# Performance work log

Hardware: AMD Instinct MI355X
Metric: run time of the kernel (lower is better)

Reference implementation:

```python
import jax, jax.numpy as jnp
import numpy as np

BN_EPS = 1e-5

def _conv1x1(w, b, x):
    # w: (O, C), b: (O,), x: (B, C, T) -> (B, O, T)
    return jnp.einsum('oc,bct->bot', w, x) + b[None, :, None]

def _maxpool2(x):
    # MaxPool1d(kernel_size=2, stride=2): (B, C, T) -> (B, C, T//2)
    B, C, T = x.shape
    return x.reshape(B, C, T // 2, 2).max(axis=-1)

def setup_inputs() -> dict:
    key = jax.random.key(0)
    ks = jax.random.split(key, 11)
    B, C, Ci, T = 4, 256, 128, 8192
    s_in = 1.0 / np.sqrt(C)
    s_ic = 1.0 / np.sqrt(Ci)
    return {
        'x':       jax.random.normal(ks[0], (B, C, T), dtype=jnp.float32),
        'theta_w': jax.random.uniform(ks[1], (Ci, C), jnp.float32, -s_in, s_in),
        'theta_b': jax.random.uniform(ks[2], (Ci,),   jnp.float32, -s_in, s_in),
        'phi_w':   jax.random.uniform(ks[3], (Ci, C), jnp.float32, -s_in, s_in),
        'phi_b':   jax.random.uniform(ks[4], (Ci,),   jnp.float32, -s_in, s_in),
        'g_w':     jax.random.uniform(ks[5], (Ci, C), jnp.float32, -s_in, s_in),
        'g_b':     jax.random.uniform(ks[6], (Ci,),   jnp.float32, -s_in, s_in),
        'w_w':     jax.random.uniform(ks[7], (C, Ci), jnp.float32, -s_ic, s_ic),
        'w_b':     jax.random.uniform(ks[8], (C,),    jnp.float32, -s_ic, s_ic),
        'gamma':   jax.random.normal(ks[9], (C,), dtype=jnp.float32),
        'beta':    jax.random.normal(ks[10], (C,), dtype=jnp.float32),
    }

def reference(x, theta_w, theta_b, phi_w, phi_b, g_w, g_b, w_w, w_b, gamma, beta):
    # x: (B, C, T)
    theta = _conv1x1(theta_w, theta_b, x)            # (B, Ci, T)
    phi   = _maxpool2(_conv1x1(phi_w, phi_b, x))     # (B, Ci, N), N = T//2
    g     = _maxpool2(_conv1x1(g_w, g_b, x))         # (B, Ci, N)
    N = phi.shape[-1]
    # f = theta^T phi / N  (dot-product similarity, divide-by-N normalization)
    f = jnp.einsum('bct,bcn->btn', theta, phi) / N   # (B, T, N)
    y = jnp.einsum('btn,bcn->bct', f, g)             # (B, Ci, T)
    wy = _conv1x1(w_w, w_b, y)                       # (B, C, T)
    # BatchNorm1d (training mode: batch statistics over (B, T), biased var)
    mean = wy.mean(axis=(0, 2), keepdims=True)
    var = ((wy - mean) ** 2).mean(axis=(0, 2), keepdims=True)
    bn = gamma[None, :, None] * (wy - mean) * jax.lax.rsqrt(var + BN_EPS) + beta[None, :, None]
    return bn + x
```

## Files before the change

### kernel.cpp

```cpp
#include <hip/hip_runtime.h>
#include <hip/hip_bf16.h>


constexpr int B = 4, C = 256, CI = 128, T = 8192, N = 4096;
constexpr int TT = 128;
constexpr int OT = 64;
constexpr int KC = 32;

constexpr size_t OFF_PHI = 0;
constexpr size_t OFF_G   = OFF_PHI + (size_t)B*CI*N;
constexpr size_t OFF_S   = OFF_G   + (size_t)B*CI*N;
constexpr size_t OFF_M   = OFF_S   + (size_t)B*CI*CI;
constexpr size_t OFF_W2  = OFF_M   + (size_t)B*C*CI;
constexpr size_t OFF_B2  = OFF_W2  + (size_t)B*C*C;
constexpr size_t OFF_WY  = OFF_B2  + (size_t)B*C;
constexpr size_t OFF_SUM = OFF_WY  + (size_t)B*C*T;
constexpr size_t OFF_A   = OFF_SUM + 2*(size_t)C;
constexpr size_t OFF_SH  = OFF_A   + (size_t)C;

__global__ __launch_bounds__(256) void k1_convpool(
    const float* __restrict__ x, const float* __restrict__ phi_w,
    const float* __restrict__ phi_b, const float* __restrict__ g_w,
    const float* __restrict__ g_b, float* __restrict__ phi_pool,
    float* __restrict__ g_pool)
{
    int t0 = blockIdx.x * TT;
    int ro = blockIdx.y * OT;
    int b  = blockIdx.z;

    __shared__ float ws_w[OT][KC];
    __shared__ float xs[KC][TT];

    int tid = threadIdx.x;
    int tx = tid & 31, ty = tid >> 5;
    float acc[8][4];
    #pragma unroll
    for (int j = 0; j < 8; ++j)
        #pragma unroll
        for (int i = 0; i < 4; ++i) acc[j][i] = 0.f;

    const float* xb = x + (size_t)b * C * T;

    for (int c0 = 0; c0 < C; c0 += KC) {
        #pragma unroll
        for (int l = 0; l < 8; ++l) {
            int li = tid + l * 256;
            int r = li >> 5, k = li & 31;
            int row = ro + r;
            ws_w[r][k] = (row < CI) ? phi_w[(size_t)row * C + c0 + k]
                                    : g_w[(size_t)(row - CI) * C + c0 + k];
        }
        #pragma unroll
        for (int l = 0; l < 16; ++l) {
            int li = tid + l * 256;
            int k = li >> 7, t = li & 127;
            xs[k][t] = xb[(size_t)(c0 + k) * T + t0 + t];
        }
        __syncthreads();
        for (int k = 0; k < KC; k += 4) {
            float4 xv0 = *reinterpret_cast<const float4*>(&xs[k + 0][tx * 4]);
            float4 xv1 = *reinterpret_cast<const float4*>(&xs[k + 1][tx * 4]);
            float4 xv2 = *reinterpret_cast<const float4*>(&xs[k + 2][tx * 4]);
            float4 xv3 = *reinterpret_cast<const float4*>(&xs[k + 3][tx * 4]);
            #pragma unroll
            for (int j = 0; j < 8; ++j) {
                float4 wv = *reinterpret_cast<const float4*>(&ws_w[ty * 8 + j][k]);
                acc[j][0] += wv.x * xv0.x; acc[j][0] += wv.y * xv1.x;
                acc[j][0] += wv.z * xv2.x; acc[j][0] += wv.w * xv3.x;
                acc[j][1] += wv.x * xv0.y; acc[j][1] += wv.y * xv1.y;
                acc[j][1] += wv.z * xv2.y; acc[j][1] += wv.w * xv3.y;
                acc[j][2] += wv.x * xv0.z; acc[j][2] += wv.y * xv1.z;
                acc[j][2] += wv.z * xv2.z; acc[j][2] += wv.w * xv3.z;
                acc[j][3] += wv.x * xv0.w; acc[j][3] += wv.y * xv1.w;
                acc[j][3] += wv.z * xv2.w; acc[j][3] += wv.w * xv3.w;
            }
        }
        __syncthreads();
    }
    int n0 = (t0 >> 1) + tx * 2;
    #pragma unroll
    for (int j = 0; j < 8; ++j) {
        int row = ro + ty * 8 + j;
        float m0 = fmaxf(acc[j][0], acc[j][1]);
        float m1 = fmaxf(acc[j][2], acc[j][3]);
        if (row < CI) {
            float bias = phi_b[row];
            float2 v = {m0 + bias, m1 + bias};
            *reinterpret_cast<float2*>(&phi_pool[((size_t)b * CI + row) * N + n0]) = v;
        } else {
            float bias = g_b[row - CI];
            float2 v = {m0 + bias, m1 + bias};
            *reinterpret_cast<float2*>(&g_pool[((size_t)b * CI + (row - CI)) * N + n0]) = v;
        }
    }
}

__global__ __launch_bounds__(256) void k2_S(
    const float* __restrict__ phi_pool, const float* __restrict__ g_pool,
    float* __restrict__ S)
{
    int n0 = blockIdx.x * 128;
    int b  = blockIdx.y;
    __shared__ float gs[CI][33];
    __shared__ float ps[CI][33];
    int tid = threadIdx.x;
    int jg = tid & 15, ig = tid >> 4;
    float acc[8][8] = {};
    const float* gp = g_pool + (size_t)b * CI * N;
    const float* pp = phi_pool + (size_t)b * CI * N;
    for (int ks = 0; ks < 128; ks += 32) {
        #pragma unroll
        for (int l = 0; l < 16; ++l) {
            int li = tid + l * 256;
            int r = li >> 5, k = li & 31;
            gs[r][k] = gp[(size_t)r * N + n0 + ks + k];
            ps[r][k] = pp[(size_t)r * N + n0 + ks + k];
        }
        __syncthreads();
        for (int k = 0; k < 32; ++k) {
            float gv[8], pv[8];
            #pragma unroll
            for (int u = 0; u < 8; ++u) gv[u] = gs[ig + 16 * u][k];
            #pragma unroll
            for (int v = 0; v < 8; ++v) pv[v] = ps[jg + 16 * v][k];
            #pragma unroll
            for (int u = 0; u < 8; ++u)
                #pragma unroll
                for (int v = 0; v < 8; ++v) acc[u][v] += gv[u] * pv[v];
        }
        __syncthreads();
    }
    #pragma unroll
    for (int u = 0; u < 8; ++u) {
        int i = ig + 16 * u;
        #pragma unroll
        for (int v = 0; v < 8; ++v) {
            int j = jg + 16 * v;
            atomicAdd(&S[((size_t)b * CI + i) * CI + j], acc[u][v]);
        }
    }
}

__global__ __launch_bounds__(256) void k3a_M(
    const float* __restrict__ w_w, const float* __restrict__ S,
    float* __restrict__ M)
{
    int idx = blockIdx.x * 256 + threadIdx.x;
    int j = idx & (CI - 1);
    int r = (idx >> 7) & (C - 1);
    int b = idx >> 15;
    const float* Sb = S + (size_t)b * CI * CI;
    float a = 0.f;
    for (int k = 0; k < CI; ++k) a += w_w[(size_t)r * CI + k] * Sb[(size_t)k * CI + j];
    M[idx] = a * (1.f / N);
}

__global__ __launch_bounds__(256) void k3b_W2(
    const float* __restrict__ M, const float* __restrict__ theta_w,
    const float* __restrict__ theta_b, const float* __restrict__ w_b,
    float* __restrict__ W2, float* __restrict__ b2)
{
    int idx = blockIdx.x * 256 + threadIdx.x;
    int c = idx & (C - 1);
    int r = (idx >> 8) & (C - 1);
    int b = idx >> 16;
    const float* Mb = M + ((size_t)b * C + r) * CI;
    float a = 0.f;
    for (int k = 0; k < CI; ++k) a += Mb[k] * theta_w[(size_t)k * C + c];
    W2[idx] = a;
    if (c == 0) {
        float bv = 0.f;
        for (int k = 0; k < CI; ++k) bv += Mb[k] * theta_b[k];
        b2[(size_t)b * C + r] = bv + w_b[r];
    }
}

__global__ __launch_bounds__(256) void k4_conv2(
    const float* __restrict__ x, const float* __restrict__ W2,
    const float* __restrict__ b2, float* __restrict__ wy,
    float* __restrict__ gsum, float* __restrict__ gsq)
{
    int t0 = blockIdx.x * TT;
    int ro = blockIdx.y * OT;
    int b  = blockIdx.z;

    __shared__ float ws_w[OT][KC];
    __shared__ float xs[KC][TT];

    int tid = threadIdx.x;
    int tx = tid & 31, ty = tid >> 5;
    float acc[8][4];
    #pragma unroll
    for (int j = 0; j < 8; ++j)
        #pragma unroll
        for (int i = 0; i < 4; ++i) acc[j][i] = 0.f;

    const float* xb  = x + (size_t)b * C * T;
    const float* W2b = W2 + (size_t)b * C * C;

    for (int c0 = 0; c0 < C; c0 += KC) {
        #pragma unroll
        for (int l = 0; l < 8; ++l) {
            int li = tid + l * 256;
            int r = li >> 5, k = li & 31;
            ws_w[r][k] = W2b[(size_t)(ro + r) * C + c0 + k];
        }
        #pragma unroll
        for (int l = 0; l < 16; ++l) {
            int li = tid + l * 256;
            int k = li >> 7, t = li & 127;
            xs[k][t] = xb[(size_t)(c0 + k) * T + t0 + t];
        }
        __syncthreads();
        for (int k = 0; k < KC; k += 4) {
            float4 xv0 = *reinterpret_cast<const float4*>(&xs[k + 0][tx * 4]);
            float4 xv1 = *reinterpret_cast<const float4*>(&xs[k + 1][tx * 4]);
            float4 xv2 = *reinterpret_cast<const float4*>(&xs[k + 2][tx * 4]);
            float4 xv3 = *reinterpret_cast<const float4*>(&xs[k + 3][tx * 4]);
            #pragma unroll
            for (int j = 0; j < 8; ++j) {
                float4 wv = *reinterpret_cast<const float4*>(&ws_w[ty * 8 + j][k]);
                acc[j][0] += wv.x * xv0.x; acc[j][0] += wv.y * xv1.x;
                acc[j][0] += wv.z * xv2.x; acc[j][0] += wv.w * xv3.x;
                acc[j][1] += wv.x * xv0.y; acc[j][1] += wv.y * xv1.y;
                acc[j][1] += wv.z * xv2.y; acc[j][1] += wv.w * xv3.y;
                acc[j][2] += wv.x * xv0.z; acc[j][2] += wv.y * xv1.z;
                acc[j][2] += wv.z * xv2.z; acc[j][2] += wv.w * xv3.z;
                acc[j][3] += wv.x * xv0.w; acc[j][3] += wv.y * xv1.w;
                acc[j][3] += wv.z * xv2.w; acc[j][3] += wv.w * xv3.w;
            }
        }
        __syncthreads();
    }
    #pragma unroll
    for (int j = 0; j < 8; ++j) {
        int row = ro + ty * 8 + j;
        float bias = b2[(size_t)b * C + row];
        float4 v;
        v.x = acc[j][0] + bias; v.y = acc[j][1] + bias;
        v.z = acc[j][2] + bias; v.w = acc[j][3] + bias;
        *reinterpret_cast<float4*>(&wy[((size_t)b * C + row) * T + t0 + tx * 4]) = v;
        float ls = v.x + v.y + v.z + v.w;
        float lq = v.x * v.x + v.y * v.y + v.z * v.z + v.w * v.w;
        #pragma unroll
        for (int m = 16; m >= 1; m >>= 1) {
            ls += __shfl_xor(ls, m, 32);
            lq += __shfl_xor(lq, m, 32);
        }
        if (tx == 0) {
            atomicAdd(&gsum[row], ls);
            atomicAdd(&gsq[row], lq);
        }
    }
}

__global__ void k4b_stats(const float* __restrict__ gsum, const float* __restrict__ gsq,
                          const float* __restrict__ gamma, const float* __restrict__ beta,
                          float* __restrict__ a, float* __restrict__ sh)
{
    int c = threadIdx.x;
    const float invBT = 1.f / (float)(B * T);
    float mean = gsum[c] * invBT;
    float var  = gsq[c] * invBT - mean * mean;
    float av = gamma[c] * rsqrtf(var + 1e-5f);
    a[c]  = av;
    sh[c] = beta[c] - av * mean;
}

__global__ __launch_bounds__(256) void k5_bn(
    const float* __restrict__ x, const float* __restrict__ wy,
    const float* __restrict__ a, const float* __restrict__ sh,
    float* __restrict__ out)
{
    size_t total4 = (size_t)B * C * T / 4;
    for (size_t i = (size_t)blockIdx.x * blockDim.x + threadIdx.x; i < total4;
         i += (size_t)gridDim.x * blockDim.x) {
        size_t e = i * 4;
        int c = (int)((e / T) % C);
        float4 w4 = reinterpret_cast<const float4*>(wy)[i];
        float4 x4 = reinterpret_cast<const float4*>(x)[i];
        float av = a[c], sv = sh[c];
        float4 o;
        o.x = av * w4.x + sv + x4.x;
        o.y = av * w4.y + sv + x4.y;
        o.z = av * w4.z + sv + x4.z;
        o.w = av * w4.w + sv + x4.w;
        reinterpret_cast<float4*>(out)[i] = o;
    }
}

extern "C" void kernel_launch(void* const* d_in, const int* in_sizes, int n_in,
                              void* d_out, int out_size, void* d_ws, size_t ws_size,
                              hipStream_t stream)
{
    const float* x       = (const float*)d_in[0];
    const float* theta_w = (const float*)d_in[1];
    const float* theta_b = (const float*)d_in[2];
    const float* phi_w   = (const float*)d_in[3];
    const float* phi_b   = (const float*)d_in[4];
    const float* g_w     = (const float*)d_in[5];
    const float* g_b     = (const float*)d_in[6];
    const float* w_w     = (const float*)d_in[7];
    const float* w_b     = (const float*)d_in[8];
    const float* gamma   = (const float*)d_in[9];
    const float* beta    = (const float*)d_in[10];
    float* out = (float*)d_out;
    float* ws  = (float*)d_ws;

    float* phi_pool = ws + OFF_PHI;
    float* g_pool   = ws + OFF_G;
    float* Sbuf     = ws + OFF_S;
    float* Mbuf     = ws + OFF_M;
    float* W2buf    = ws + OFF_W2;
    float* b2buf    = ws + OFF_B2;
    float* wybuf    = ws + OFF_WY;
    float* gsum     = ws + OFF_SUM;
    float* gsq      = gsum + C;
    float* abuf     = ws + OFF_A;
    float* shbuf    = ws + OFF_SH;

    hipMemsetAsync(Sbuf, 0, (size_t)B * CI * CI * sizeof(float), stream);
    hipMemsetAsync(gsum, 0, 2 * (size_t)C * sizeof(float), stream);

    k1_convpool<<<dim3(T / TT, C / OT, B), 256, 0, stream>>>(
        x, phi_w, phi_b, g_w, g_b, phi_pool, g_pool);
    k2_S<<<dim3(N / 128, B), 256, 0, stream>>>(phi_pool, g_pool, Sbuf);
    k3a_M<<<(B * C * CI) / 256, 256, 0, stream>>>(w_w, Sbuf, Mbuf);
    k3b_W2<<<(B * C * C) / 256, 256, 0, stream>>>(Mbuf, theta_w, theta_b, w_b, W2buf, b2buf);
    k4_conv2<<<dim3(T / TT, C / OT, B), 256, 0, stream>>>(
        x, W2buf, b2buf, wybuf, gsum, gsq);
    k4b_stats<<<1, C, 0, stream>>>(gsum, gsq, gamma, beta, abuf, shbuf);
    k5_bn<<<2048, 256, 0, stream>>>(x, wybuf, abuf, shbuf, out);
}
```

Before: 299.9 us.

## Move 1x1 convs and Gram matrix to bf16x3 split MFMA with recomputed output

Replaces the FP32 FMA GEMMs (conv+pool, phi·g Gram reduction, final conv) with MFMA bf16 instructions, using a hi/lo bf16 split and three MFMAs per product to keep near-FP32 accuracy. x is transposed and split once into bf16 hi/lo in a pre-pass, and the pooled phi/g outputs are stored the same way. The wy intermediate is removed: the final conv runs twice, first to gather BN statistics and then again to apply BN and the residual directly to the output. This trades redundant MFMA work and an extra split pass for fewer FP32 ALU cycles and less wy global traffic.

```diff
diff --git a/kernel.cpp b/kernel.cpp
--- a/kernel.cpp
+++ b/kernel.cpp
@@ -2,148 +2,230 @@
 #include <hip/hip_bf16.h>
 
 
-constexpr int B = 4, C = 256, CI = 128, T = 8192, N = 4096;
-constexpr int TT = 128;
-constexpr int OT = 64;
-constexpr int KC = 32;
-
-constexpr size_t OFF_PHI = 0;
-constexpr size_t OFF_G   = OFF_PHI + (size_t)B*CI*N;
-constexpr size_t OFF_S   = OFF_G   + (size_t)B*CI*N;
-constexpr size_t OFF_M   = OFF_S   + (size_t)B*CI*CI;
-constexpr size_t OFF_W2  = OFF_M   + (size_t)B*C*CI;
-constexpr size_t OFF_B2  = OFF_W2  + (size_t)B*C*C;
-constexpr size_t OFF_WY  = OFF_B2  + (size_t)B*C;
-constexpr size_t OFF_SUM = OFF_WY  + (size_t)B*C*T;
-constexpr size_t OFF_A   = OFF_SUM + 2*(size_t)C;
-constexpr size_t OFF_SH  = OFF_A   + (size_t)C;
-
-__global__ __launch_bounds__(256) void k1_convpool(
-    const float* __restrict__ x, const float* __restrict__ phi_w,
-    const float* __restrict__ phi_b, const float* __restrict__ g_w,
-    const float* __restrict__ g_b, float* __restrict__ phi_pool,
-    float* __restrict__ g_pool)
-{
-    int t0 = blockIdx.x * TT;
-    int ro = blockIdx.y * OT;
-    int b  = blockIdx.z;
-
-    __shared__ float ws_w[OT][KC];
-    __shared__ float xs[KC][TT];
-
+constexpr int B = 4, C = 256, CI = 128, T = 8192, NN = 4096;
+
+using s16x8 = __attribute__((ext_vector_type(8))) short;
+using f32x4 = __attribute__((ext_vector_type(4))) float;
+
+__device__ __forceinline__ unsigned short f2bf(float f) {
+    unsigned int x = __float_as_uint(f);
+    unsigned int r = (x + 0x7fffu + ((x >> 16) & 1u)) >> 16;
+    return (unsigned short)r;
+}
+__device__ __forceinline__ float bf2f(unsigned short u) {
+    return __uint_as_float((unsigned int)u << 16);
+}
+
+#define MFMA(a, b, c) __builtin_amdgcn_mfma_f32_16x16x32_bf16((a), (b), (c), 0, 0, 0)
+
+constexpr size_t SZ_XT = (size_t)B * T * C * 2;
+constexpr size_t O_XTH = 0;
+constexpr size_t O_XTL = O_XTH + SZ_XT;
+constexpr size_t O_WSH = O_XTL + SZ_XT;
+constexpr size_t O_WSL = O_WSH + (size_t)C * C * 2;
+constexpr size_t SZ_P  = (size_t)B * CI * NN * 2;
+constexpr size_t O_PH  = O_WSL + (size_t)C * C * 2;
+constexpr size_t O_PL  = O_PH + SZ_P;
+constexpr size_t O_GH  = O_PL + SZ_P;
+constexpr size_t O_GL  = O_GH + SZ_P;
+constexpr size_t O_S   = O_GL + SZ_P;
+constexpr size_t O_M   = O_S  + (size_t)B * CI * CI * 4;
+constexpr size_t O_W2H = O_M  + (size_t)B * C * CI * 4;
+constexpr size_t O_W2L = O_W2H + (size_t)B * C * C * 2;
+constexpr size_t O_B2  = O_W2L + (size_t)B * C * C * 2;
+constexpr size_t O_GS  = O_B2 + (size_t)B * C * 4;
+constexpr size_t O_GQ  = O_GS + (size_t)C * 4;
+constexpr size_t O_A   = O_GQ + (size_t)C * 4;
+constexpr size_t O_SH  = O_A  + (size_t)C * 4;
+
+__global__ __launch_bounds__(256) void k0_split(
+    const float* __restrict__ x, unsigned short* __restrict__ xth,
+    unsigned short* __restrict__ xtl)
+{
+    __shared__ float xs[64][65];
+    int t0 = blockIdx.x * 64, c0 = blockIdx.y * 64, b = blockIdx.z;
     int tid = threadIdx.x;
-    int tx = tid & 31, ty = tid >> 5;
-    float acc[8][4];
-    #pragma unroll
-    for (int j = 0; j < 8; ++j)
-        #pragma unroll
-        for (int i = 0; i < 4; ++i) acc[j][i] = 0.f;
-
     const float* xb = x + (size_t)b * C * T;
-
-    for (int c0 = 0; c0 < C; c0 += KC) {
-        #pragma unroll
-        for (int l = 0; l < 8; ++l) {
-            int li = tid + l * 256;
-            int r = li >> 5, k = li & 31;
-            int row = ro + r;
-            ws_w[r][k] = (row < CI) ? phi_w[(size_t)row * C + c0 + k]
-                                    : g_w[(size_t)(row - CI) * C + c0 + k];
-        }
-        #pragma unroll
-        for (int l = 0; l < 16; ++l) {
-            int li = tid + l * 256;
-            int k = li >> 7, t = li & 127;
-            xs[k][t] = xb[(size_t)(c0 + k) * T + t0 + t];
-        }
-        __syncthreads();
-        for (int k = 0; k < KC; k += 4) {
-            float4 xv0 = *reinterpret_cast<const float4*>(&xs[k + 0][tx * 4]);
-            float4 xv1 = *reinterpret_cast<const float4*>(&xs[k + 1][tx * 4]);
-            float4 xv2 = *reinterpret_cast<const float4*>(&xs[k + 2][tx * 4]);
-            float4 xv3 = *reinterpret_cast<const float4*>(&xs[k + 3][tx * 4]);
-            #pragma unroll
-            for (int j = 0; j < 8; ++j) {
-                float4 wv = *reinterpret_cast<const float4*>(&ws_w[ty * 8 + j][k]);
-                acc[j][0] += wv.x * xv0.x; acc[j][0] += wv.y * xv1.x;
-                acc[j][0] += wv.z * xv2.x; acc[j][0] += wv.w * xv3.x;
-                acc[j][1] += wv.x * xv0.y; acc[j][1] += wv.y * xv1.y;
-                acc[j][1] += wv.z * xv2.y; acc[j][1] += wv.w * xv3.y;
-                acc[j][2] += wv.x * xv0.z; acc[j][2] += wv.y * xv1.z;
-                acc[j][2] += wv.z * xv2.z; acc[j][2] += wv.w * xv3.z;
-                acc[j][3] += wv.x * xv0.w; acc[j][3] += wv.y * xv1.w;
-                acc[j][3] += wv.z * xv2.w; acc[j][3] += wv.w * xv3.w;
+    #pragma unroll
+    for (int p = 0; p < 4; ++p) {
+        int idx = tid + p * 256;
+        int cr = idx >> 4;
+        int tg = (idx & 15) * 4;
+        float4 v = *reinterpret_cast<const float4*>(xb + (size_t)(c0 + cr) * T + t0 + tg);
+        xs[tg + 0][cr] = v.x; xs[tg + 1][cr] = v.y;
+        xs[tg + 2][cr] = v.z; xs[tg + 3][cr] = v.w;
+    }
+    __syncthreads();
+    #pragma unroll
+    for (int p = 0; p < 2; ++p) {
+        int idx = tid + p * 256;
+        int cg = idx & 7, tl = idx >> 3;
+        s16x8 hs, ls;
+        #pragma unroll
+        for (int j = 0; j < 8; ++j) {
+            float v = xs[tl][cg * 8 + j];
+            unsigned short h = f2bf(v);
+            unsigned short l = f2bf(v - bf2f(h));
+            hs[j] = (short)h; ls[j] = (short)l;
+        }
+        size_t dst = ((size_t)b * T + t0 + tl) * C + c0 + cg * 8;
+        *reinterpret_cast<s16x8*>(xth + dst) = hs;
+        *reinterpret_cast<s16x8*>(xtl + dst) = ls;
+    }
+}
+
+__global__ __launch_bounds__(256) void k0w(
+    const float* __restrict__ phi_w, const float* __restrict__ g_w,
+    unsigned short* __restrict__ wsh, unsigned short* __restrict__ wsl)
+{
+    int idx = blockIdx.x * 256 + threadIdx.x;
+    int row = idx >> 8, c = idx & 255;
+    float v = (row < CI) ? phi_w[(size_t)row * C + c] : g_w[(size_t)(row - CI) * C + c];
+    unsigned short h = f2bf(v);
+    wsh[idx] = h;
+    wsl[idx] = f2bf(v - bf2f(h));
+}
+
+__global__ __launch_bounds__(512) void k1_mfma(
+    const unsigned short* __restrict__ xth, const unsigned short* __restrict__ xtl,
+    const unsigned short* __restrict__ wsh, const unsigned short* __restrict__ wsl,
+    const float* __restrict__ phi_b, const float* __restrict__ g_b,
+    unsigned short* __restrict__ ph, unsigned short* __restrict__ pl,
+    unsigned short* __restrict__ gh, unsigned short* __restrict__ gl)
+{
+    int b = blockIdx.y, t0 = blockIdx.x * 128;
+    int tid = threadIdx.x, lane = tid & 63, w = tid >> 6;
+    int wo = w & 3, th = w >> 2;
+    int lr = lane & 15, lk = lane >> 4;
+
+    f32x4 acc[4][4];
+    #pragma unroll
+    for (int i = 0; i < 4; ++i)
+        #pragma unroll
+        for (int j = 0; j < 4; ++j) acc[i][j] = (f32x4){0.f, 0.f, 0.f, 0.f};
+
+    const unsigned short* ah_b = xth + ((size_t)b * T + t0 + th * 64 + lr) * C + lk * 8;
+    const unsigned short* al_b = xtl + ((size_t)b * T + t0 + th * 64 + lr) * C + lk * 8;
+    const unsigned short* bh_b = wsh + (size_t)(wo * 64 + lr) * C + lk * 8;
+    const unsigned short* bl_b = wsl + (size_t)(wo * 64 + lr) * C + lk * 8;
+
+    for (int c0 = 0; c0 < C; c0 += 32) {
+        s16x8 Ah[4], Al[4], Bh[4], Bl[4];
+        #pragma unroll
+        for (int ts = 0; ts < 4; ++ts) {
+            Ah[ts] = *reinterpret_cast<const s16x8*>(ah_b + (size_t)ts * 16 * C + c0);
+            Al[ts] = *reinterpret_cast<const s16x8*>(al_b + (size_t)ts * 16 * C + c0);
+        }
+        #pragma unroll
+        for (int os = 0; os < 4; ++os) {
+            Bh[os] = *reinterpret_cast<const s16x8*>(bh_b + (size_t)os * 16 * C + c0);
+            Bl[os] = *reinterpret_cast<const s16x8*>(bl_b + (size_t)os * 16 * C + c0);
+        }
+        #pragma unroll
+        for (int os = 0; os < 4; ++os)
+            #pragma unroll
+            for (int ts = 0; ts < 4; ++ts) {
+                acc[os][ts] = MFMA(Ah[ts], Bh[os], acc[os][ts]);
+                acc[os][ts] = MFMA(Al[ts], Bh[os], acc[os][ts]);
+                acc[os][ts] = MFMA(Ah[ts], Bl[os], acc[os][ts]);
             }
-        }
-        __syncthreads();
-    }
-    int n0 = (t0 >> 1) + tx * 2;
-    #pragma unroll
-    for (int j = 0; j < 8; ++j) {
-        int row = ro + ty * 8 + j;
-        float m0 = fmaxf(acc[j][0], acc[j][1]);
-        float m1 = fmaxf(acc[j][2], acc[j][3]);
-        if (row < CI) {
-            float bias = phi_b[row];
-            float2 v = {m0 + bias, m1 + bias};
-            *reinterpret_cast<float2*>(&phi_pool[((size_t)b * CI + row) * N + n0]) = v;
-        } else {
-            float bias = g_b[row - CI];
-            float2 v = {m0 + bias, m1 + bias};
-            *reinterpret_cast<float2*>(&g_pool[((size_t)b * CI + (row - CI)) * N + n0]) = v;
-        }
-    }
-}
-
-__global__ __launch_bounds__(256) void k2_S(
-    const float* __restrict__ phi_pool, const float* __restrict__ g_pool,
+    }
+
+    __shared__ unsigned int pool_s[256][65];
+    #pragma unroll
+    for (int os = 0; os < 4; ++os) {
+        int o = wo * 64 + os * 16 + lr;
+        float bias = (o < CI) ? phi_b[o] : g_b[o - CI];
+        #pragma unroll
+        for (int ts = 0; ts < 4; ++ts) {
+            f32x4 v = acc[os][ts];
+            float m0 = fmaxf(v[0], v[1]) + bias;
+            float m1 = fmaxf(v[2], v[3]) + bias;
+            int nl = th * 32 + ts * 8 + lk * 2;
+            unsigned short h0 = f2bf(m0), h1 = f2bf(m1);
+            unsigned int u0 = (unsigned int)h0 | ((unsigned int)f2bf(m0 - bf2f(h0)) << 16);
+            unsigned int u1 = (unsigned int)h1 | ((unsigned int)f2bf(m1 - bf2f(h1)) << 16);
+            pool_s[o][nl] = u0;
+            pool_s[o][nl + 1] = u1;
+        }
+    }
+    __syncthreads();
+    int o = tid >> 1, hf = tid & 1;
+    size_t n0 = (size_t)(t0 >> 1) + hf * 32;
+    unsigned short* dh = (o < CI ? ph + ((size_t)b * CI + o) * NN
+                                 : gh + ((size_t)b * CI + o - CI) * NN) + n0;
+    unsigned short* dl = (o < CI ? pl + ((size_t)b * CI + o) * NN
+                                 : gl + ((size_t)b * CI + o - CI) * NN) + n0;
+    #pragma unroll
+    for (int g4 = 0; g4 < 4; ++g4) {
+        s16x8 hs, ls;
+        #pragma unroll
+        for (int j = 0; j < 8; ++j) {
+            unsigned int u = pool_s[o][hf * 32 + g4 * 8 + j];
+            hs[j] = (short)(u & 0xffffu);
+            ls[j] = (short)(u >> 16);
+        }
+        *reinterpret_cast<s16x8*>(dh + g4 * 8) = hs;
+        *reinterpret_cast<s16x8*>(dl + g4 * 8) = ls;
+    }
+}
+
+__global__ __launch_bounds__(256) void k2_mfma(
+    const unsigned short* __restrict__ ph, const unsigned short* __restrict__ pl,
+    const unsigned short* __restrict__ gh, const unsigned short* __restrict__ gl,
     float* __restrict__ S)
 {
-    int n0 = blockIdx.x * 128;
-    int b  = blockIdx.y;
-    __shared__ float gs[CI][33];
-    __shared__ float ps[CI][33];
-    int tid = threadIdx.x;
-    int jg = tid & 15, ig = tid >> 4;
-    float acc[8][8] = {};
-    const float* gp = g_pool + (size_t)b * CI * N;
-    const float* pp = phi_pool + (size_t)b * CI * N;
-    for (int ks = 0; ks < 128; ks += 32) {
-        #pragma unroll
-        for (int l = 0; l < 16; ++l) {
-            int li = tid + l * 256;
-            int r = li >> 5, k = li & 31;
-            gs[r][k] = gp[(size_t)r * N + n0 + ks + k];
-            ps[r][k] = pp[(size_t)r * N + n0 + ks + k];
-        }
-        __syncthreads();
-        for (int k = 0; k < 32; ++k) {
-            float gv[8], pv[8];
-            #pragma unroll
-            for (int u = 0; u < 8; ++u) gv[u] = gs[ig + 16 * u][k];
-            #pragma unroll
-            for (int v = 0; v < 8; ++v) pv[v] = ps[jg + 16 * v][k];
-            #pragma unroll
-            for (int u = 0; u < 8; ++u)
-                #pragma unroll
-                for (int v = 0; v < 8; ++v) acc[u][v] += gv[u] * pv[v];
-        }
-        __syncthreads();
-    }
-    #pragma unroll
-    for (int u = 0; u < 8; ++u) {
-        int i = ig + 16 * u;
-        #pragma unroll
-        for (int v = 0; v < 8; ++v) {
-            int j = jg + 16 * v;
-            atomicAdd(&S[((size_t)b * CI + i) * CI + j], acc[u][v]);
+    int b = blockIdx.y, n0 = blockIdx.x * 512;
+    int tid = threadIdx.x, lane = tid & 63, w = tid >> 6;
+    int lr = lane & 15, lk = lane >> 4;
+
+    f32x4 acc[2][8];
+    #pragma unroll
+    for (int i = 0; i < 2; ++i)
+        #pragma unroll
+        for (int j = 0; j < 8; ++j) acc[i][j] = (f32x4){0.f, 0.f, 0.f, 0.f};
+
+    const unsigned short* ah_b = gh + ((size_t)b * CI + w * 32 + lr) * NN + n0 + lk * 8;
+    const unsigned short* al_b = gl + ((size_t)b * CI + w * 32 + lr) * NN + n0 + lk * 8;
+    const unsigned short* bh_b = ph + ((size_t)b * CI + lr) * NN + n0 + lk * 8;
+    const unsigned short* bl_b = pl + ((size_t)b * CI + lr) * NN + n0 + lk * 8;
+
+    for (int ks = 0; ks < 16; ++ks) {
+        s16x8 Ah[2], Al[2], Bh[8], Bl[8];
+        #pragma unroll
+        for (int is = 0; is < 2; ++is) {
+            Ah[is] = *reinterpret_cast<const s16x8*>(ah_b + (size_t)is * 16 * NN + ks * 32);
+            Al[is] = *reinterpret_cast<const s16x8*>(al_b + (size_t)is * 16 * NN + ks * 32);
+        }
+        #pragma unroll
+        for (int js = 0; js < 8; ++js) {
+            Bh[js] = *reinterpret_cast<const s16x8*>(bh_b + (size_t)js * 16 * NN + ks * 32);
+            Bl[js] = *reinterpret_cast<const s16x8*>(bl_b + (size_t)js * 16 * NN + ks * 32);
+        }
+        #pragma unroll
+        for (int is = 0; is < 2; ++is)
+            #pragma unroll
+            for (int js = 0; js < 8; ++js) {
+                acc[is][js] = MFMA(Ah[is], Bh[js], acc[is][js]);
+                acc[is][js] = MFMA(Al[is], Bh[js], acc[is][js]);
+                acc[is][js] = MFMA(Ah[is], Bl[js], acc[is][js]);
+            }
+    }
+    #pragma unroll
+    for (int is = 0; is < 2; ++is) {
+        int i0 = w * 32 + is * 16 + lk * 4;
+        #pragma unroll
+        for (int js = 0; js < 8; ++js) {
+            int j = js * 16 + lr;
+            #pragma unroll
+            for (int r = 0; r < 4; ++r)
+                atomicAdd(&S[((size_t)b * CI + i0 + r) * CI + j], acc[is][js][r]);
         }
     }
 }
 
 __global__ __launch_bounds__(256) void k3a_M(
-    const float* __restrict__ w_w, const float* __restrict__ S,
-    float* __restrict__ M)
+    const float* __restrict__ w_w, const float* __restrict__ S, float* __restrict__ M)
 {
     int idx = blockIdx.x * 256 + threadIdx.x;
     int j = idx & (CI - 1);
@@ -152,13 +234,14 @@
     const float* Sb = S + (size_t)b * CI * CI;
     float a = 0.f;
     for (int k = 0; k < CI; ++k) a += w_w[(size_t)r * CI + k] * Sb[(size_t)k * CI + j];
-    M[idx] = a * (1.f / N);
+    M[idx] = a * (1.f / NN);
 }
 
 __global__ __launch_bounds__(256) void k3b_W2(
     const float* __restrict__ M, const float* __restrict__ theta_w,
     const float* __restrict__ theta_b, const float* __restrict__ w_b,
-    float* __restrict__ W2, float* __restrict__ b2)
+    unsigned short* __restrict__ w2h, unsigned short* __restrict__ w2l,
+    float* __restrict__ b2)
 {
     int idx = blockIdx.x * 256 + threadIdx.x;
     int c = idx & (C - 1);
@@ -167,7 +250,9 @@
     const float* Mb = M + ((size_t)b * C + r) * CI;
     float a = 0.f;
     for (int k = 0; k < CI; ++k) a += Mb[k] * theta_w[(size_t)k * C + c];
-    W2[idx] = a;
+    unsigned short h = f2bf(a);
+    w2h[idx] = h;
+    w2l[idx] = f2bf(a - bf2f(h));
     if (c == 0) {
         float bv = 0.f;
         for (int k = 0; k < CI; ++k) bv += Mb[k] * theta_b[k];
@@ -175,81 +260,82 @@
     }
 }
 
-__global__ __launch_bounds__(256) void k4_conv2(
-    const float* __restrict__ x, const float* __restrict__ W2,
-    const float* __restrict__ b2, float* __restrict__ wy,
-    float* __restrict__ gsum, float* __restrict__ gsq)
-{
-    int t0 = blockIdx.x * TT;
-    int ro = blockIdx.y * OT;
-    int b  = blockIdx.z;
-
-    __shared__ float ws_w[OT][KC];
-    __shared__ float xs[KC][TT];
-
-    int tid = threadIdx.x;
-    int tx = tid & 31, ty = tid >> 5;
-    float acc[8][4];
-    #pragma unroll
-    for (int j = 0; j < 8; ++j)
-        #pragma unroll
-        for (int i = 0; i < 4; ++i) acc[j][i] = 0.f;
-
-    const float* xb  = x + (size_t)b * C * T;
-    const float* W2b = W2 + (size_t)b * C * C;
-
-    for (int c0 = 0; c0 < C; c0 += KC) {
-        #pragma unroll
-        for (int l = 0; l < 8; ++l) {
-            int li = tid + l * 256;
-            int r = li >> 5, k = li & 31;
-            ws_w[r][k] = W2b[(size_t)(ro + r) * C + c0 + k];
-        }
-        #pragma unroll
-        for (int l = 0; l < 16; ++l) {
-            int li = tid + l * 256;
-            int k = li >> 7, t = li & 127;
-            xs[k][t] = xb[(size_t)(c0 + k) * T + t0 + t];
-        }
-        __syncthreads();
-        for (int k = 0; k < KC; k += 4) {
-            float4 xv0 = *reinterpret_cast<const float4*>(&xs[k + 0][tx * 4]);
-            float4 xv1 = *reinterpret_cast<const float4*>(&xs[k + 1][tx * 4]);
-            float4 xv2 = *reinterpret_cast<const float4*>(&xs[k + 2][tx * 4]);
-            float4 xv3 = *reinterpret_cast<const float4*>(&xs[k + 3][tx * 4]);
-            #pragma unroll
-            for (int j = 0; j < 8; ++j) {
-                float4 wv = *reinterpret_cast<const float4*>(&ws_w[ty * 8 + j][k]);
-                acc[j][0] += wv.x * xv0.x; acc[j][0] += wv.y * xv1.x;
-                acc[j][0] += wv.z * xv2.x; acc[j][0] += wv.w * xv3.x;
-                acc[j][1] += wv.x * xv0.y; acc[j][1] += wv.y * xv1.y;
-                acc[j][1] += wv.z * xv2.y; acc[j][1] += wv.w * xv3.y;
-                acc[j][2] += wv.x * xv0.z; acc[j][2] += wv.y * xv1.z;
-                acc[j][2] += wv.z * xv2.z; acc[j][2] += wv.w * xv3.z;
-                acc[j][3] += wv.x * xv0.w; acc[j][3] += wv.y * xv1.w;
-                acc[j][3] += wv.z * xv2.w; acc[j][3] += wv.w * xv3.w;
+template <int MODE>
+__global__ __launch_bounds__(512) void k45_mfma(
+    const unsigned short* __restrict__ xth, const unsigned short* __restrict__ xtl,
+    const unsigned short* __restrict__ w2h, const unsigned short* __restrict__ w2l,
+    const float* __restrict__ b2, const float* __restrict__ x,
+    const float* __restrict__ abuf, const float* __restrict__ shbuf,
+    float* __restrict__ gsum, float* __restrict__ gsq, float* __restrict__ out)
+{
+    int b = blockIdx.y, t0 = blockIdx.x * 128;
+    int tid = threadIdx.x, lane = tid & 63, w = tid >> 6;
+    int wo = w & 3, th = w >> 2;
+    int lr = lane & 15, lk = lane >> 4;
+
+    f32x4 acc[4][4];
+    #pragma unroll
+    for (int i = 0; i < 4; ++i)
+        #pragma unroll
+        for (int j = 0; j < 4; ++j) acc[i][j] = (f32x4){0.f, 0.f, 0.f, 0.f};
+
+    const unsigned short* ah_b = xth + ((size_t)b * T + t0 + th * 64 + lr) * C + lk * 8;
+    const unsigned short* al_b = xtl + ((size_t)b * T + t0 + th * 64 + lr) * C + lk * 8;
+    const unsigned short* bh_b = w2h + (size_t)b * C * C + (size_t)(wo * 64 + lr) * C + lk * 8;
+    const unsigned short* bl_b = w2l + (size_t)b * C * C + (size_t)(wo * 64 + lr) * C + lk * 8;
+
+    for (int c0 = 0; c0 < C; c0 += 32) {
+        s16x8 Ah[4], Al[4], Bh[4], Bl[4];
+        #pragma unroll
+        for (int ts = 0; ts < 4; ++ts) {
+            Ah[ts] = *reinterpret_cast<const s16x8*>(ah_b + (size_t)ts * 16 * C + c0);
+            Al[ts] = *reinterpret_cast<const s16x8*>(al_b + (size_t)ts * 16 * C + c0);
+        }
+        #pragma unroll
+        for (int os = 0; os < 4; ++os) {
+            Bh[os] = *reinterpret_cast<const s16x8*>(bh_b + (size_t)os * 16 * C + c0);
+            Bl[os] = *reinterpret_cast<const s16x8*>(bl_b + (size_t)os * 16 * C + c0);
+        }
+        #pragma unroll
+        for (int os = 0; os < 4; ++os)
+            #pragma unroll
+            for (int ts = 0; ts < 4; ++ts) {
+                acc[os][ts] = MFMA(Ah[ts], Bh[os], acc[os][ts]);
+                acc[os][ts] = MFMA(Al[ts], Bh[os], acc[os][ts]);
+                acc[os][ts] = MFMA(Ah[ts], Bl[os], acc[os][ts]);
             }
-        }
-        __syncthreads();
-    }
-    #pragma unroll
-    for (int j = 0; j < 8; ++j) {
-        int row = ro + ty * 8 + j;
-        float bias = b2[(size_t)b * C + row];
-        float4 v;
-        v.x = acc[j][0] + bias; v.y = acc[j][1] + bias;
-        v.z = acc[j][2] + bias; v.w = acc[j][3] + bias;
-        *reinterpret_cast<float4*>(&wy[((size_t)b * C + row) * T + t0 + tx * 4]) = v;
-        float ls = v.x + v.y + v.z + v.w;
-        float lq = v.x * v.x + v.y * v.y + v.z * v.z + v.w * v.w;
-        #pragma unroll
-        for (int m = 16; m >= 1; m >>= 1) {
-            ls += __shfl_xor(ls, m, 32);
-            lq += __shfl_xor(lq, m, 32);
-        }
-        if (tx == 0) {
-            atomicAdd(&gsum[row], ls);
-            atomicAdd(&gsq[row], lq);
+    }
+
+    #pragma unroll
+    for (int os = 0; os < 4; ++os) {
+        int o = wo * 64 + os * 16 + lr;
+        float bv = b2[(size_t)b * C + o];
+        if (MODE == 0) {
+            float s = 0.f, q = 0.f;
+            #pragma unroll
+            for (int ts = 0; ts < 4; ++ts)
+                #pragma unroll
+                for (int r = 0; r < 4; ++r) {
+                    float v = acc[os][ts][r] + bv;
+                    s += v; q += v * v;
+                }
+            s += __shfl_xor(s, 16); s += __shfl_xor(s, 32);
+            q += __shfl_xor(q, 16); q += __shfl_xor(q, 32);
+            if (lk == 0) { atomicAdd(&gsum[o], s); atomicAdd(&gsq[o], q); }
+        } else {
+            float av = abuf[o], sv = shbuf[o];
+            #pragma unroll
+            for (int ts = 0; ts < 4; ++ts) {
+                int t = t0 + th * 64 + ts * 16 + lk * 4;
+                size_t base = ((size_t)b * C + o) * T + t;
+                float4 xv = *reinterpret_cast<const float4*>(x + base);
+                float4 ov;
+                ov.x = av * (acc[os][ts][0] + bv) + sv + xv.x;
+                ov.y = av * (acc[os][ts][1] + bv) + sv + xv.y;
+                ov.z = av * (acc[os][ts][2] + bv) + sv + xv.z;
+                ov.w = av * (acc[os][ts][3] + bv) + sv + xv.w;
+                *reinterpret_cast<float4*>(out + base) = ov;
+            }
         }
     }
 }
@@ -265,28 +351,6 @@
     float av = gamma[c] * rsqrtf(var + 1e-5f);
     a[c]  = av;
     sh[c] = beta[c] - av * mean;
-}
-
-__global__ __launch_bounds__(256) void k5_bn(
-    const float* __restrict__ x, const float* __restrict__ wy,
-    const float* __restrict__ a, const float* __restrict__ sh,
-    float* __restrict__ out)
-{
-    size_t total4 = (size_t)B * C * T / 4;
-    for (size_t i = (size_t)blockIdx.x * blockDim.x + threadIdx.x; i < total4;
-         i += (size_t)gridDim.x * blockDim.x) {
-        size_t e = i * 4;
-        int c = (int)((e / T) % C);
-        float4 w4 = reinterpret_cast<const float4*>(wy)[i];
-        float4 x4 = reinterpret_cast<const float4*>(x)[i];
-        float av = a[c], sv = sh[c];
-        float4 o;
-        o.x = av * w4.x + sv + x4.x;
-        o.y = av * w4.y + sv + x4.y;
-        o.z = av * w4.z + sv + x4.z;
-        o.w = av * w4.w + sv + x4.w;
-        reinterpret_cast<float4*>(out)[i] = o;
-    }
 }
 
 extern "C" void kernel_launch(void* const* d_in, const int* in_sizes, int n_in,
@@ -305,30 +369,40 @@
     const float* gamma   = (const float*)d_in[9];
     const float* beta    = (const float*)d_in[10];
     float* out = (float*)d_out;
-    float* ws  = (float*)d_ws;
-
-    float* phi_pool = ws + OFF_PHI;
-    float* g_pool   = ws + OFF_G;
-    float* Sbuf     = ws + OFF_S;
-    float* Mbuf     = ws + OFF_M;
-    float* W2buf    = ws + OFF_W2;
-    float* b2buf    = ws + OFF_B2;
-    float* wybuf    = ws + OFF_WY;
-    float* gsum     = ws + OFF_SUM;
-    float* gsq      = gsum + C;
-    float* abuf     = ws + OFF_A;
-    float* shbuf    = ws + OFF_SH;
+    char* ws = (char*)d_ws;
+
+    unsigned short* xth = (unsigned short*)(ws + O_XTH);
+    unsigned short* xtl = (unsigned short*)(ws + O_XTL);
+    unsigned short* wsh = (unsigned short*)(ws + O_WSH);
+    unsigned short* wsl = (unsigned short*)(ws + O_WSL);
+    unsigned short* ph  = (unsigned short*)(ws + O_PH);
+    unsigned short* pl  = (unsigned short*)(ws + O_PL);
+    unsigned short* gh  = (unsigned short*)(ws + O_GH);
+    unsigned short* gl  = (unsigned short*)(ws + O_GL);
+    float* Sbuf  = (float*)(ws + O_S);
+    float* Mbuf  = (float*)(ws + O_M);
+    unsigned short* w2h = (unsigned short*)(ws + O_W2H);
+    unsigned short* w2l = (unsigned short*)(ws + O_W2L);
+    float* b2    = (float*)(ws + O_B2);
+    float* gsum  = (float*)(ws + O_GS);
+    float* gsq   = (float*)(ws + O_GQ);
+    float* abuf  = (float*)(ws + O_A);
+    float* shbuf = (float*)(ws + O_SH);
 
     hipMemsetAsync(Sbuf, 0, (size_t)B * CI * CI * sizeof(float), stream);
     hipMemsetAsync(gsum, 0, 2 * (size_t)C * sizeof(float), stream);
 
-    k1_convpool<<<dim3(T / TT, C / OT, B), 256, 0, stream>>>(
-        x, phi_w, phi_b, g_w, g_b, phi_pool, g_pool);
-    k2_S<<<dim3(N / 128, B), 256, 0, stream>>>(phi_pool, g_pool, Sbuf);
-    k3a_M<<<(B * C * CI) / 256, 256, 0, stream>>>(w_w, Sbuf, Mbuf);
-    k3b_W2<<<(B * C * C) / 256, 256, 0, stream>>>(Mbuf, theta_w, theta_b, w_b, W2buf, b2buf);
-    k4_conv2<<<dim3(T / TT, C / OT, B), 256, 0, stream>>>(
-        x, W2buf, b2buf, wybuf, gsum, gsq);
+    k0_split<<<dim3(T / 64, C / 64, B), 256, 0, stream>>>(x, xth, xtl);
+    k0w<<<dim3(C * C / 256), 256, 0, stream>>>(phi_w, g_w, wsh, wsl);
+    k1_mfma<<<dim3(T / 128, B), 512, 0, stream>>>(xth, xtl, wsh, wsl, phi_b, g_b,
+                                                  ph, pl, gh, gl);
+    k2_mfma<<<dim3(NN / 512, B), 256, 0, stream>>>(ph, pl, gh, gl, Sbuf);
+    k3a_M<<<dim3(B * C * CI / 256), 256, 0, stream>>>(w_w, Sbuf, Mbuf);
+    k3b_W2<<<dim3(B * C * C / 256), 256, 0, stream>>>(Mbuf, theta_w, theta_b, w_b,
+                                                      w2h, w2l, b2);
+    k45_mfma<0><<<dim3(T / 128, B), 512, 0, stream>>>(xth, xtl, w2h, w2l, b2, x,
+                                                      abuf, shbuf, gsum, gsq, out);
     k4b_stats<<<1, C, 0, stream>>>(gsum, gsq, gamma, beta, abuf, shbuf);
-    k5_bn<<<2048, 256, 0, stream>>>(x, wybuf, abuf, shbuf, out);
-}
+    k45_mfma<1><<<dim3(T / 128, B), 512, 0, stream>>>(xth, xtl, w2h, w2l, b2, x,
+                                                      abuf, shbuf, gsum, gsq, out);
+}
```

Measured after the change: 284.2 us. 1.06x faster.
